# Performance work log

Hardware: AMD Instinct MI355X
Metric: run time of the kernel (lower is better)

## Reference

```python
import jax, jax.numpy as jnp
import numpy as np

D = 1024
H = 16
HD = D // H
S = 2048
B = 4
EPS = 1e-5


def gelu_tanh(x):
    c = jnp.sqrt(2.0 / jnp.pi).astype(x.dtype)
    return 0.5 * x * (1.0 + jnp.tanh(c * (x + 0.044715 * x ** 3)))


def layernorm(x, gamma, beta):
    mu = jnp.mean(x, axis=-1, keepdims=True)
    var = jnp.var(x, axis=-1, keepdims=True)
    return (x - mu) * jax.lax.rsqrt(var + EPS) * gamma + beta


def setup_inputs() -> dict:
    key = jax.random.key(0)
    ks = jax.random.split(key, 12)
    s = 0.02
    return {
        "x": jax.random.normal(ks[0], (B, S, D), jnp.float32),
        "Wq": jax.random.normal(ks[1], (D, D), jnp.float32) * s,
        "Wk": jax.random.normal(ks[2], (D, D), jnp.float32) * s,
        "Wv": jax.random.normal(ks[3], (D, D), jnp.float32) * s,
        "Wo": jax.random.normal(ks[4], (D, D), jnp.float32) * s,
        "bo": jnp.zeros((D,), jnp.float32),
        "W1": jax.random.normal(ks[5], (D, 4 * D), jnp.float32) * s,
        "b1": jnp.zeros((4 * D,), jnp.float32),
        "W2": jax.random.normal(ks[6], (4 * D, D), jnp.float32) * s,
        "b2": jnp.zeros((D,), jnp.float32),
        "g1": jnp.ones((D,), jnp.float32),
        "be1": jnp.zeros((D,), jnp.float32),
        "g2": jnp.ones((D,), jnp.float32),
        "be2": jnp.zeros((D,), jnp.float32),
    }


def reference(x, Wq, Wk, Wv, Wo, bo, W1, b1, W2, b2, g1, be1, g2, be2):
    b, n, d = x.shape
    # --- attention sub-block (pre-LN) ---
    h = layernorm(x, g1, be1)
    q = (h @ Wq).reshape(b, n, H, HD).transpose(0, 2, 1, 3)  # [b,H,n,hd]
    k = (h @ Wk).reshape(b, n, H, HD).transpose(0, 2, 1, 3)
    v = (h @ Wv).reshape(b, n, H, HD).transpose(0, 2, 1, 3)
    scores = jnp.einsum('bhqd,bhkd->bhqk', q, k) / jnp.sqrt(jnp.float32(HD))
    causal = jnp.tril(jnp.ones((n, n), dtype=bool))
    scores = jnp.where(causal, scores, -jnp.inf)
    w = jax.nn.softmax(scores, axis=-1)  # dropout rate 0 -> identity
    attn = jnp.einsum('bhqk,bhkd->bhqd', w, v)
    attn = attn.transpose(0, 2, 1, 3).reshape(b, n, d)
    x = x + (attn @ Wo + bo)
    # --- FFN sub-block (pre-LN) ---
    h = layernorm(x, g2, be2)
    h = gelu_tanh(h @ W1 + b1) @ W2 + b2
    return x + h
```

## Files before the change

### kernel.cpp

```cpp
#include <hip/hip_runtime.h>
#include <hip/hip_bf16.h>
#include <math.h>


typedef __attribute__((ext_vector_type(8))) short bf16x8;
typedef __attribute__((ext_vector_type(4))) float f32x4;

#define AS1 __attribute__((address_space(1)))
#define AS3 __attribute__((address_space(3)))

__device__ __forceinline__ void gl_lds16(const void* g, void* l) {
  __builtin_amdgcn_global_load_lds((const AS1 void*)g, (AS3 void*)l, 16, 0, 0);
}

__device__ __forceinline__ float gelu_f(float x) {
  const float c = 0.7978845608028654f;
  const float y = c * (x + 0.044715f * x * x * x);
  const float ay = fabsf(y);
  const float e = __expf(-2.0f * ay);
  float t = (1.0f - e) / (1.0f + e);
  t = copysignf(t, y);
  return 0.5f * x * (1.0f + t);
}

__device__ __forceinline__ float bf2f(short s) {
  unsigned u = ((unsigned)(unsigned short)s) << 16;
  return __builtin_bit_cast(float, u);
}
__device__ __forceinline__ short f2bf(float f) {
  __hip_bfloat16 h = __float2bfloat16(f);
  return __builtin_bit_cast(short, h);
}

__global__ void __launch_bounds__(256) tcvt_all(
    const float* __restrict__ Wq, const float* __restrict__ Wk,
    const float* __restrict__ Wv, const float* __restrict__ Wo,
    const float* __restrict__ W1, const float* __restrict__ W2,
    __hip_bfloat16* __restrict__ WqkvT, __hip_bfloat16* __restrict__ WoT,
    __hip_bfloat16* __restrict__ W1T, __hip_bfloat16* __restrict__ W2T) {
  __shared__ float t[32][33];
  const int bid = blockIdx.x;
  const float* W;
  __hip_bfloat16* WT;
  int K, N, n0, k0;
  if (bid < 4096) {
    const int which = bid >> 10, r = bid & 1023;
    K = 1024; N = 1024;
    n0 = (r & 31) * 32; k0 = (r >> 5) * 32;
    W = which == 0 ? Wq : which == 1 ? Wk : which == 2 ? Wv : Wo;
    WT = which < 3 ? WqkvT + which * 1024 * 1024 : WoT;
  } else if (bid < 8192) {
    const int r = bid - 4096;
    K = 1024; N = 4096;
    n0 = (r & 127) * 32; k0 = (r >> 7) * 32;
    W = W1; WT = W1T;
  } else {
    const int r = bid - 8192;
    K = 4096; N = 1024;
    n0 = (r & 31) * 32; k0 = (r >> 5) * 32;
    W = W2; WT = W2T;
  }
  const int tx = threadIdx.x, ty0 = threadIdx.y;
#pragma unroll
  for (int i = 0; i < 4; i++) {
    int ty = ty0 + i * 8;
    t[ty][tx] = W[(size_t)(k0 + ty) * N + n0 + tx];
  }
  __syncthreads();
#pragma unroll
  for (int i = 0; i < 4; i++) {
    int ty = ty0 + i * 8;
    WT[(size_t)(n0 + ty) * K + k0 + tx] = __float2bfloat16(t[tx][ty]);
  }
}

__global__ void __launch_bounds__(256) vtr_kernel(
    const __hip_bfloat16* __restrict__ qkv, __hip_bfloat16* __restrict__ vt) {
  __shared__ __hip_bfloat16 t[32][33];
  const int s0 = blockIdx.x * 32;
  const int hd0 = blockIdx.y * 32;
  const int bh = blockIdx.z;
  const int b = bh >> 4, h = bh & 15;
  const int tx = threadIdx.x, ty0 = threadIdx.y;
  const __hip_bfloat16* src =
      qkv + (size_t)(b * 2048 + s0) * 3072 + 2048 + h * 64 + hd0;
#pragma unroll
  for (int i = 0; i < 4; i++) {
    int ty = ty0 + i * 8;
    t[ty][tx] = src[(size_t)ty * 3072 + tx];
  }
  __syncthreads();
  __hip_bfloat16* dst = vt + ((size_t)bh * 64 + hd0) * 2048 + s0;
#pragma unroll
  for (int i = 0; i < 4; i++) {
    int ty = ty0 + i * 8;
    dst[(size_t)ty * 2048 + tx] = t[tx][ty];
  }
}

__global__ void __launch_bounds__(256) ln_kernel(
    const float* __restrict__ x, const float* __restrict__ gma,
    const float* __restrict__ bta, __hip_bfloat16* __restrict__ out) {
  const int row = blockIdx.x;
  const int tid = threadIdx.x;
  const float4 v = ((const float4*)(x + (size_t)row * 1024))[tid];
  float s = v.x + v.y + v.z + v.w;
  float s2 = v.x * v.x + v.y * v.y + v.z * v.z + v.w * v.w;
#pragma unroll
  for (int m = 32; m; m >>= 1) {
    s += __shfl_xor(s, m);
    s2 += __shfl_xor(s2, m);
  }
  __shared__ float red[8];
  const int w = tid >> 6, lane = tid & 63;
  if (lane == 0) { red[w] = s; red[4 + w] = s2; }
  __syncthreads();
  s = red[0] + red[1] + red[2] + red[3];
  s2 = red[4] + red[5] + red[6] + red[7];
  const float mu = s * (1.0f / 1024.0f);
  const float var = s2 * (1.0f / 1024.0f) - mu * mu;
  const float rs = rsqrtf(var + 1e-5f);
  const float4 gv = ((const float4*)gma)[tid];
  const float4 bv = ((const float4*)bta)[tid];
  __hip_bfloat16* orow = out + (size_t)row * 1024 + tid * 4;
  orow[0] = __float2bfloat16((v.x - mu) * rs * gv.x + bv.x);
  orow[1] = __float2bfloat16((v.y - mu) * rs * gv.y + bv.y);
  orow[2] = __float2bfloat16((v.z - mu) * rs * gv.z + bv.z);
  orow[3] = __float2bfloat16((v.w - mu) * rs * gv.w + bv.w);
}

__global__ void __launch_bounds__(256) ln_bf16_kernel(
    const __hip_bfloat16* __restrict__ x, const float* __restrict__ gma,
    const float* __restrict__ bta, __hip_bfloat16* __restrict__ out) {
  const int row = blockIdx.x;
  const int tid = threadIdx.x;
  const short4 raw = ((const short4*)(x + (size_t)row * 1024))[tid];
  const float v0 = bf2f(raw.x), v1 = bf2f(raw.y), v2 = bf2f(raw.z),
              v3 = bf2f(raw.w);
  float s = v0 + v1 + v2 + v3;
  float s2 = v0 * v0 + v1 * v1 + v2 * v2 + v3 * v3;
#pragma unroll
  for (int m = 32; m; m >>= 1) {
    s += __shfl_xor(s, m);
    s2 += __shfl_xor(s2, m);
  }
  __shared__ float red[8];
  const int w = tid >> 6, lane = tid & 63;
  if (lane == 0) { red[w] = s; red[4 + w] = s2; }
  __syncthreads();
  s = red[0] + red[1] + red[2] + red[3];
  s2 = red[4] + red[5] + red[6] + red[7];
  const float mu = s * (1.0f / 1024.0f);
  const float var = s2 * (1.0f / 1024.0f) - mu * mu;
  const float rs = rsqrtf(var + 1e-5f);
  const float4 gv = ((const float4*)gma)[tid];
  const float4 bv = ((const float4*)bta)[tid];
  __hip_bfloat16* orow = out + (size_t)row * 1024 + tid * 4;
  orow[0] = __float2bfloat16((v0 - mu) * rs * gv.x + bv.x);
  orow[1] = __float2bfloat16((v1 - mu) * rs * gv.y + bv.y);
  orow[2] = __float2bfloat16((v2 - mu) * rs * gv.z + bv.z);
  orow[3] = __float2bfloat16((v3 - mu) * rs * gv.w + bv.w);
}

template <int BM, int BN, int EPI>
__global__ void __launch_bounds__(512, 2) gemm8(
    const __hip_bfloat16* __restrict__ Ap, const __hip_bfloat16* __restrict__ Bp,
    void* __restrict__ outp, const float* __restrict__ bias,
    const float* __restrict__ resid, int N, int K) {
  constexpr int PM = BM / 2;
  constexpr int MR = PM / 16;
  constexpr int NPH = MR / 2;
  constexpr int HA = BM / 128;
  constexpr int ABYTES = BM * 128;
  constexpr int BUFB = ABYTES + BN * 128;
  __shared__ __attribute__((aligned(128))) char smem[2 * BUFB];

  const int tid = threadIdx.x;
  const int lane = tid & 63, w = tid >> 6;
  const int wr = w >> 2, wc = w & 3;
  const int cr = lane & 15, g = lane >> 4;

  const int gx = gridDim.x;
  const int nwg = gx * gridDim.y;
  const int orig = blockIdx.y * gx + blockIdx.x;
  const int f = (orig & 7) * (nwg >> 3) + (orig >> 3);
  const int sid = f >> 4, wit = f & 15;
  const int stm = gx >> 2;
  const int bm = (sid % stm) * 4 + (wit & 3);
  const int bn = (sid / stm) * 4 + (wit >> 2);
  const int bmr = bm * BM, bnr = bn * BN;
  const int nkt = K >> 6;

  const int srow8 = lane >> 3;
  const int ssl = ((lane & 7) ^ srow8) * 8;
  unsigned aofs[2][2], bofs[2][2];
#pragma unroll
  for (int h = 0; h < 2; h++)
#pragma unroll
    for (int c = 0; c < 2; c++) {
      const int ha = (h < HA) ? h : 0;
      aofs[h][c] =
          (unsigned)(((bmr + ha * 128 + (w + c * 8) * 8 + srow8) * K + ssl) * 2);
      bofs[h][c] =
          (unsigned)(((bnr + h * 128 + (w + c * 8) * 8 + srow8) * K + ssl) * 2);
    }

  const int rk = cr & 7;
  const char* aP[2][2];
  const char* bP[2][2];
#pragma unroll
  for (int bf = 0; bf < 2; bf++)
#pragma unroll
    for (int ks = 0; ks < 2; ks++) {
      aP[bf][ks] =
          smem + bf * BUFB + (wr * PM + cr) * 128 + ((ks * 4 + g) ^ rk) * 16;
      bP[bf][ks] = smem + bf * BUFB + ABYTES + (wc * 64 + cr) * 128 +
                   ((ks * 4 + g) ^ rk) * 16;
    }

#define STG_A(BUF, tt, h)                                                     \
  do {                                                                        \
    const unsigned col = (unsigned)(tt) * 128u;                               \
    gl_lds16((const char*)Ap + aofs[h][0] + col,                              \
             smem + (BUF) * BUFB + (h) * 16384 + w * 1024);                   \
    gl_lds16((const char*)Ap + aofs[h][1] + col,                              \
             smem + (BUF) * BUFB + (h) * 16384 + (w + 8) * 1024);             \
  } while (0)
#define STG_B(BUF, tt, h)                                                     \
  do {                                                                        \
    const unsigned col = (unsigned)(tt) * 128u;                               \
    gl_lds16((const char*)Bp + bofs[h][0] + col,                              \
             smem + (BUF) * BUFB + ABYTES + (h) * 16384 + w * 1024);          \
    gl_lds16((const char*)Bp + bofs[h][1] + col,                              \
             smem + (BUF) * BUFB + ABYTES + (h) * 16384 + (w + 8) * 1024);    \
  } while (0)

  f32x4 acc[MR][4];
#pragma unroll
  for (int i = 0; i < MR; i++)
#pragma unroll
    for (int j = 0; j < 4; j++) acc[i][j] = (f32x4){0.f, 0.f, 0.f, 0.f};
  bf16x8 bv[4][2];

#pragma unroll
  for (int h = 0; h < HA; h++) STG_A(0, 0, h);
  STG_B(0, 0, 0); STG_B(0, 0, 1);
  STG_B(1, 1, 0); STG_B(1, 1, 1);

#define TILE_BODY(BUF, t)                                                     \
  {                                                                           \
    asm volatile("s_waitcnt vmcnt(4)" ::: "memory");                          \
    __builtin_amdgcn_s_barrier();                                             \
    const int tA = ((t) + 1 < nkt) ? (t) + 1 : (t) - 1;                       \
    const int tB = ((t) + 2 < nkt) ? (t) + 2 : (t);                           \
    _Pragma("unroll") for (int q = 0; q < NPH; q++) {                         \
      bf16x8 av[2][2];                                                        \
      _Pragma("unroll") for (int mm = 0; mm < 2; mm++)                        \
          _Pragma("unroll") for (int ks = 0; ks < 2; ks++) av[mm][ks] =       \
          *(const bf16x8*)(aP[BUF][ks] + (q * 2 + mm) * 2048);                \
      if (q == 0) {                                                           \
        _Pragma("unroll") for (int n = 0; n < 4; n++)                         \
            _Pragma("unroll") for (int ks = 0; ks < 2; ks++) bv[n][ks] =      \
            *(const bf16x8*)(bP[BUF][ks] + n * 2048);                         \
      }                                                                       \
      if constexpr (NPH == 4) {                                               \
        if (q == 0) { STG_A((BUF) ^ 1, tA, 0); }                              \
        else if (q == 1) { STG_A((BUF) ^ 1, tA, 1); }                         \
        else if (q == 2) { STG_B(BUF, tB, 0); }                               \
        else { STG_B(BUF, tB, 1); }                                           \
      } else {                                                                \
        if (q == 0) { STG_A((BUF) ^ 1, tA, 0); }                              \
        else { STG_B(BUF, tB, 0); STG_B(BUF, tB, 1); }                        \
      }                                                                       \
      __builtin_amdgcn_s_barrier();                                           \
      asm volatile("s_waitcnt lgkmcnt(0)" ::: "memory");                      \
      __builtin_amdgcn_s_setprio(1);                                          \
      _Pragma("unroll") for (int mm = 0; mm < 2; mm++)                        \
          _Pragma("unroll") for (int n = 0; n < 4; n++)                       \
              _Pragma("unroll") for (int ks = 0; ks < 2; ks++)                \
                  acc[q * 2 + mm][n] =                                        \
          __builtin_amdgcn_mfma_f32_16x16x32_bf16(av[mm][ks], bv[n][ks],      \
                                                  acc[q * 2 + mm][n], 0, 0, 0); \
      __builtin_amdgcn_s_setprio(0);                                          \
    }                                                                         \
  }

  for (int t = 0; t < nkt; t += 2) {
    TILE_BODY(0, t)
    TILE_BODY(1, t + 1)
  }
  asm volatile("s_waitcnt vmcnt(0)" ::: "memory");

#pragma unroll
  for (int m = 0; m < MR; m++) {
#pragma unroll
    for (int rr = 0; rr < 4; rr++) {
      const int row = bmr + wr * PM + m * 16 + g * 4 + rr;
#pragma unroll
      for (int n = 0; n < 4; n++) {
        const int col = bnr + wc * 64 + n * 16 + cr;
        float v = acc[m][n][rr];
        if (EPI == 0) {
          ((__hip_bfloat16*)outp)[(size_t)row * N + col] = __float2bfloat16(v);
        } else if (EPI == 2) {
          v = gelu_f(v + bias[col]);
          ((__hip_bfloat16*)outp)[(size_t)row * N + col] = __float2bfloat16(v);
        } else {
          v += bias[col] + resid[(size_t)row * N + col];
          ((__hip_bfloat16*)outp)[(size_t)row * N + col] = __float2bfloat16(v);
        }
      }
    }
  }
#undef STG_A
#undef STG_B
#undef TILE_BODY
}

template <int EPI>
__global__ void __launch_bounds__(256) gemm97(
    const __hip_bfloat16* __restrict__ Ap, const __hip_bfloat16* __restrict__ Bp,
    void* __restrict__ outp, const float* __restrict__ bias,
    const void* __restrict__ resid, int N, int K) {
  __shared__ __hip_bfloat16 sA[128 * 64];
  __shared__ __hip_bfloat16 sB[128 * 64];
  const int tid = threadIdx.x;
  const int lane = tid & 63, w = tid >> 6;
  const int wr = w >> 1, wc = w & 1;
  const int cr = lane & 15, g = lane >> 4;

  const int gx = gridDim.x;
  const int nwg = gx * gridDim.y;
  const int orig = blockIdx.y * gx + blockIdx.x;
  const int f = (orig & 7) * (nwg >> 3) + (orig >> 3);
  const int sid = f >> 4, wit = f & 15;
  const int stm = gx >> 2;
  const int bm = (sid % stm) * 4 + (wit & 3);
  const int bn = (sid / stm) * 4 + (wit >> 2);
  const int bmr = bm * 128, bnr = bn * 128;

  const int l8 = lane >> 3;
  const int ssl = ((lane & 7) ^ l8) * 8;
  const int rk = cr & 7;

  f32x4 acc[4][4];
#pragma unroll
  for (int i = 0; i < 4; i++)
#pragma unroll
    for (int j = 0; j < 4; j++) acc[i][j] = (f32x4){0.f, 0.f, 0.f, 0.f};

  for (int k0 = 0; k0 < K; k0 += 64) {
#pragma unroll
    for (int i = 0; i < 4; i++) {
      const int chunk = w * 4 + i;
      const int row = chunk * 8 + l8;
      gl_lds16(Ap + (size_t)(bmr + row) * K + k0 + ssl, sA + chunk * 512);
      gl_lds16(Bp + (size_t)(bnr + row) * K + k0 + ssl, sB + chunk * 512);
    }
    __syncthreads();
#pragma unroll
    for (int ks = 0; ks < 2; ks++) {
      bf16x8 a[4], b[4];
#pragma unroll
      for (int m = 0; m < 4; m++)
        a[m] = *(const bf16x8*)(sA + (wr * 64 + m * 16 + cr) * 64 +
                                ((ks * 4 + g) ^ rk) * 8);
#pragma unroll
      for (int n = 0; n < 4; n++)
        b[n] = *(const bf16x8*)(sB + (wc * 64 + n * 16 + cr) * 64 +
                                ((ks * 4 + g) ^ rk) * 8);
#pragma unroll
      for (int m = 0; m < 4; m++)
#pragma unroll
        for (int n = 0; n < 4; n++)
          acc[m][n] =
              __builtin_amdgcn_mfma_f32_16x16x32_bf16(a[m], b[n], acc[m][n], 0, 0, 0);
    }
    __syncthreads();
  }

#pragma unroll
  for (int m = 0; m < 4; m++) {
#pragma unroll
    for (int rr = 0; rr < 4; rr++) {
      const int row = bmr + wr * 64 + m * 16 + g * 4 + rr;
#pragma unroll
      for (int n = 0; n < 4; n++) {
        const int col = bnr + wc * 64 + n * 16 + cr;
        float v = acc[m][n][rr];
        if (EPI == 0) {
          ((__hip_bfloat16*)outp)[(size_t)row * N + col] = __float2bfloat16(v);
        } else if (EPI == 1) {
          v += bias[col] + ((const float*)resid)[(size_t)row * N + col];
          ((float*)outp)[(size_t)row * N + col] = v;
        } else {
          v += bias[col] +
               bf2f(((const short*)resid)[(size_t)row * N + col]);
          ((float*)outp)[(size_t)row * N + col] = v;
        }
      }
    }
  }
}

__global__ void __launch_bounds__(256) attn_kernel(
    const __hip_bfloat16* __restrict__ qkv, const __hip_bfloat16* __restrict__ vt,
    __hip_bfloat16* __restrict__ o) {
  __shared__ __hip_bfloat16 sK[2][64 * 64];
  __shared__ __hip_bfloat16 sV[2][64 * 64];
  __shared__ __hip_bfloat16 pl[4][16][64];
  const int tid = threadIdx.x, lane = tid & 63, w = tid >> 6;
  const int orig = blockIdx.x;
  const int f = (orig & 7) * 64 + (orig >> 3);
  const int bh = f >> 3;
  const int p = f & 7;
  const int b = bh >> 4, h = bh & 15;
  const int cr = lane & 15, g = lane >> 4;
  const float NEG = -1e30f;
  const float SC2 = 0.18033688011112042f;
  const int sw = cr & 7;
  const int sg0 = (g ^ sw) * 8;
  const int sg1 = ((g ^ sw) ^ 4) * 8;
  const int pkey = (cr & 7) << 1;

  bf16x8 vones;
#pragma unroll
  for (int j = 0; j < 8; j++) vones[j] = (short)0x3F80;

  const __hip_bfloat16* kbase = qkv + (size_t)(b * 2048) * 3072 + 1024 + h * 64;
  const __hip_bfloat16* vbase = vt + (size_t)bh * 64 * 2048;
  const int l8 = lane >> 3, c8 = lane & 7;
  const int c8s = (c8 ^ l8) * 8;
#define STAGE_TILE(bi, ktile)                                                   \
  {                                                                             \
    _Pragma("unroll") for (int i = 0; i < 2; i++) {                             \
      const int rb = (i * 4 + w) * 8 + l8;                                      \
      gl_lds16(kbase + (size_t)((ktile) * 64 + rb) * 3072 + c8s,                \
               &sK[bi][(i * 4 + w) * 512]);                                     \
      gl_lds16(vbase + (size_t)rb * 2048 + (ktile) * 64 + c8s,                  \
               &sV[bi][(i * 4 + w) * 512]);                                     \
    }                                                                           \
  }

  for (int seg = 0; seg < 2; ++seg) {
    const int qt = seg == 0 ? (15 - p) : p;
    const int qr0 = qt * 128 + w * 32;

    bf16x8 aq[2][2];
#pragma unroll
    for (int m = 0; m < 2; m++) {
      const __hip_bfloat16* qp =
          qkv + (size_t)(b * 2048 + qr0 + m * 16 + cr) * 3072 + h * 64 + g * 8;
      bf16x8 q0 = *(const bf16x8*)qp;
      bf16x8 q1 = *(const bf16x8*)(qp + 32);
#pragma unroll
      for (int j = 0; j < 8; j++) {
        aq[m][0][j] = f2bf(bf2f(q0[j]) * SC2);
        aq[m][1][j] = f2bf(bf2f(q1[j]) * SC2);
      }
    }

    f32x4 oacc[2][4];
    f32x4 lacc[2];
#pragma unroll
    for (int m = 0; m < 2; m++) {
#pragma unroll
      for (int i = 0; i < 4; i++) oacc[m][i] = (f32x4){0.f, 0.f, 0.f, 0.f};
      lacc[m] = (f32x4){0.f, 0.f, 0.f, 0.f};
    }

    const int nkt = (qt + 1) * 2;
    __syncthreads();
    STAGE_TILE(0, 0);
    asm volatile("s_waitcnt vmcnt(0)" ::: "memory");
    __syncthreads();
    int cur = 0;

    for (int kt = 0; kt < nkt; ++kt) {
      if (kt + 1 < nkt) STAGE_TILE(cur ^ 1, kt + 1);

      if (kt * 64 <= qr0 + 31) {
        f32x4 st[4][2];
        __builtin_amdgcn_s_setprio(1);
#pragma unroll
        for (int kf = 0; kf < 4; kf++) {
          const bf16x8 bk0 = *(const bf16x8*)&sK[cur][(kf * 16 + cr) * 64 + sg0];
          const bf16x8 bk1 = *(const bf16x8*)&sK[cur][(kf * 16 + cr) * 64 + sg1];
#pragma unroll
          for (int mq = 0; mq < 2; mq++) {
            f32x4 z = (f32x4){0.f, 0.f, 0.f, 0.f};
            z = __builtin_amdgcn_mfma_f32_16x16x32_bf16(bk0, aq[mq][0], z, 0, 0, 0);
            z = __builtin_amdgcn_mfma_f32_16x16x32_bf16(bk1, aq[mq][1], z, 0, 0, 0);
            st[kf][mq] = z;
          }
        }
        __builtin_amdgcn_s_setprio(0);
        if (kt * 64 + 63 > qr0) {
#pragma unroll
          for (int kf = 0; kf < 4; kf++)
#pragma unroll
            for (int mq = 0; mq < 2; mq++)
#pragma unroll
              for (int rr = 0; rr < 4; rr++) {
                const int kvcol = kt * 64 + kf * 16 + g * 4 + rr;
                const int qrow = qr0 + mq * 16 + cr;
                if (kvcol > qrow) st[kf][mq][rr] = NEG;
              }
        }
        bf16x8 bvv0[4], bvv1[4];
#pragma unroll
        for (int nf = 0; nf < 4; nf++) {
          bvv0[nf] = *(const bf16x8*)&sV[cur][(nf * 16 + cr) * 64 + sg0];
          bvv1[nf] = *(const bf16x8*)&sV[cur][(nf * 16 + cr) * 64 + sg1];
        }
#pragma unroll
        for (int mq = 0; mq < 2; mq++) {
#pragma unroll
          for (int kf = 0; kf < 4; kf++) {
            unsigned pb[4];
#pragma unroll
            for (int rr = 0; rr < 4; rr++) {
              const float pv = exp2f(st[kf][mq][rr]);
              pb[rr] = __builtin_bit_cast(unsigned, pv) & 0xFFFF0000u;
            }
            uint2 pk;
            pk.x = pb[1] | (pb[0] >> 16);
            pk.y = pb[3] | (pb[2] >> 16);
            const int slot4 = (kf * 4 + g) ^ pkey;
            *(uint2*)&pl[w][cr][slot4 * 4] = pk;
          }
          const bf16x8 pa0 = *(const bf16x8*)&pl[w][cr][((2 * g) ^ pkey) * 4];
          const bf16x8 pa1 = *(const bf16x8*)&pl[w][cr][((2 * g + 8) ^ pkey) * 4];
          __builtin_amdgcn_s_setprio(1);
#pragma unroll
          for (int nf = 0; nf < 4; nf++) {
            oacc[mq][nf] = __builtin_amdgcn_mfma_f32_16x16x32_bf16(pa0, bvv0[nf], oacc[mq][nf], 0, 0, 0);
            oacc[mq][nf] = __builtin_amdgcn_mfma_f32_16x16x32_bf16(pa1, bvv1[nf], oacc[mq][nf], 0, 0, 0);
          }
          lacc[mq] = __builtin_amdgcn_mfma_f32_16x16x32_bf16(pa0, vones, lacc[mq], 0, 0, 0);
          lacc[mq] = __builtin_amdgcn_mfma_f32_16x16x32_bf16(pa1, vones, lacc[mq], 0, 0, 0);
          __builtin_amdgcn_s_setprio(0);
        }
      }

      if (kt + 1 < nkt) {
        asm volatile("s_waitcnt vmcnt(0)" ::: "memory");
        __syncthreads();
        cur ^= 1;
      }
    }

#pragma unroll
    for (int m = 0; m < 2; m++) {
      float il[4];
#pragma unroll
      for (int rr = 0; rr < 4; rr++)
        il[rr] = 1.0f / lacc[m][rr];
#pragma unroll
      for (int nf = 0; nf < 4; nf++)
#pragma unroll
        for (int rr = 0; rr < 4; rr++) {
          const int row = qr0 + m * 16 + g * 4 + rr;
          o[(size_t)(b * 2048 + row) * 1024 + h * 64 + nf * 16 + cr] =
              __float2bfloat16(oacc[m][nf][rr] * il[rr]);
        }
    }
  }
#undef STAGE_TILE
}

extern "C" void kernel_launch(void* const* d_in, const int* in_sizes, int n_in,
                              void* d_out, int out_size, void* d_ws, size_t ws_size,
                              hipStream_t stream) {
  const float* x   = (const float*)d_in[0];
  const float* Wq  = (const float*)d_in[1];
  const float* Wk  = (const float*)d_in[2];
  const float* Wv  = (const float*)d_in[3];
  const float* Wo  = (const float*)d_in[4];
  const float* bo  = (const float*)d_in[5];
  const float* W1  = (const float*)d_in[6];
  const float* b1  = (const float*)d_in[7];
  const float* W2  = (const float*)d_in[8];
  const float* b2  = (const float*)d_in[9];
  const float* g1  = (const float*)d_in[10];
  const float* be1 = (const float*)d_in[11];
  const float* g2  = (const float*)d_in[12];
  const float* be2 = (const float*)d_in[13];

  char* ws = (char*)d_ws;
  const size_t MB = 1024 * 1024;
  __hip_bfloat16* hA    = (__hip_bfloat16*)(ws + 0);
  __hip_bfloat16* attnO = (__hip_bfloat16*)(ws + 0);
  __hip_bfloat16* qkv   = (__hip_bfloat16*)(ws + 16 * MB);
  __hip_bfloat16* x2b   = (__hip_bfloat16*)(ws + 16 * MB);
  __hip_bfloat16* h2    = (__hip_bfloat16*)(ws + 48 * MB);
  __hip_bfloat16* vtg   = (__hip_bfloat16*)(ws + 64 * MB);
  __hip_bfloat16* act   = (__hip_bfloat16*)(ws + 64 * MB);
  __hip_bfloat16* WqkvT = (__hip_bfloat16*)(ws + 128 * MB);
  __hip_bfloat16* WoT   = (__hip_bfloat16*)(ws + 134 * MB);
  __hip_bfloat16* W1T   = (__hip_bfloat16*)(ws + 136 * MB);
  __hip_bfloat16* W2T   = (__hip_bfloat16*)(ws + 144 * MB);

  const dim3 tb(32, 8);
  tcvt_all<<<12288, tb, 0, stream>>>(Wq, Wk, Wv, Wo, W1, W2,
                                     WqkvT, WoT, W1T, W2T);

  ln_kernel<<<8192, 256, 0, stream>>>(x, g1, be1, hA);
  gemm8<128, 256, 0><<<dim3(64, 12), 512, 0, stream>>>(
      hA, WqkvT, qkv, nullptr, nullptr, 3072, 1024);
  vtr_kernel<<<dim3(64, 2, 64), tb, 0, stream>>>(qkv, vtg);
  attn_kernel<<<512, 256, 0, stream>>>(qkv, vtg, attnO);
  gemm8<128, 256, 3><<<dim3(64, 4), 512, 0, stream>>>(
      attnO, WoT, x2b, bo, x, 1024, 1024);
  ln_bf16_kernel<<<8192, 256, 0, stream>>>(x2b, g2, be2, h2);
  gemm8<256, 256, 2><<<dim3(32, 16), 512, 0, stream>>>(
      h2, W1T, act, b1, nullptr, 4096, 1024);
  gemm97<4><<<dim3(64, 8), 256, 0, stream>>>(
      act, W2T, (float*)d_out, b2, x2b, 1024, 4096);
  (void)in_sizes; (void)n_in; (void)out_size; (void)ws_size;
}
```

Baseline: 364.1 us.

## Fuse V transpose into QKV GEMM epilogue and move W1 GEMM to gemm97

The QKV projection GEMM now writes the V part directly in transposed [b, hd, s] layout from its accumulators, using packed 4-element stores, so the separate vtr_kernel launch and its extra read/write of V go away. The FFN up-projection with GELU is also switched from the 512-thread gemm8<256,256> kernel to the 256-thread gemm97 kernel with a GELU epilogue. That swap changes the tile shape and grid for the largest GEMM and could help or hurt its throughput. The transposed stores are strided across rows of the output, so they may coalesce poorly.

```diff
diff --git a/kernel.cpp b/kernel.cpp
--- a/kernel.cpp
+++ b/kernel.cpp
@@ -74,30 +74,6 @@
   }
 }
 
-__global__ void __launch_bounds__(256) vtr_kernel(
-    const __hip_bfloat16* __restrict__ qkv, __hip_bfloat16* __restrict__ vt) {
-  __shared__ __hip_bfloat16 t[32][33];
-  const int s0 = blockIdx.x * 32;
-  const int hd0 = blockIdx.y * 32;
-  const int bh = blockIdx.z;
-  const int b = bh >> 4, h = bh & 15;
-  const int tx = threadIdx.x, ty0 = threadIdx.y;
-  const __hip_bfloat16* src =
-      qkv + (size_t)(b * 2048 + s0) * 3072 + 2048 + h * 64 + hd0;
-#pragma unroll
-  for (int i = 0; i < 4; i++) {
-    int ty = ty0 + i * 8;
-    t[ty][tx] = src[(size_t)ty * 3072 + tx];
-  }
-  __syncthreads();
-  __hip_bfloat16* dst = vt + ((size_t)bh * 64 + hd0) * 2048 + s0;
-#pragma unroll
-  for (int i = 0; i < 4; i++) {
-    int ty = ty0 + i * 8;
-    dst[(size_t)ty * 2048 + tx] = t[tx][ty];
-  }
-}
-
 __global__ void __launch_bounds__(256) ln_kernel(
     const float* __restrict__ x, const float* __restrict__ gma,
     const float* __restrict__ bta, __hip_bfloat16* __restrict__ out) {
@@ -166,7 +142,8 @@
 __global__ void __launch_bounds__(512, 2) gemm8(
     const __hip_bfloat16* __restrict__ Ap, const __hip_bfloat16* __restrict__ Bp,
     void* __restrict__ outp, const float* __restrict__ bias,
-    const float* __restrict__ resid, int N, int K) {
+    const float* __restrict__ resid, int N, int K,
+    __hip_bfloat16* __restrict__ vtp) {
   constexpr int PM = BM / 2;
   constexpr int MR = PM / 16;
   constexpr int NPH = MR / 2;
@@ -291,6 +268,26 @@
   }
   asm volatile("s_waitcnt vmcnt(0)" ::: "memory");
 
+  if (EPI == 5 && bnr >= 2048) {
+    const int bq = bmr >> 11;
+    const int sbase = (bmr & 2047) + wr * PM + g * 4;
+#pragma unroll
+    for (int m = 0; m < MR; m++) {
+      const int s0 = sbase + m * 16;
+#pragma unroll
+      for (int n = 0; n < 4; n++) {
+        const int hdg = bnr - 2048 + wc * 64 + n * 16 + cr;
+        short4 pk;
+        pk.x = f2bf(acc[m][n][0]);
+        pk.y = f2bf(acc[m][n][1]);
+        pk.z = f2bf(acc[m][n][2]);
+        pk.w = f2bf(acc[m][n][3]);
+        *(short4*)&vtp[((size_t)bq * 1024 + hdg) * 2048 + s0] = pk;
+      }
+    }
+    return;
+  }
+
 #pragma unroll
   for (int m = 0; m < MR; m++) {
 #pragma unroll
@@ -300,10 +297,7 @@
       for (int n = 0; n < 4; n++) {
         const int col = bnr + wc * 64 + n * 16 + cr;
         float v = acc[m][n][rr];
-        if (EPI == 0) {
-          ((__hip_bfloat16*)outp)[(size_t)row * N + col] = __float2bfloat16(v);
-        } else if (EPI == 2) {
-          v = gelu_f(v + bias[col]);
+        if (EPI == 0 || EPI == 5) {
           ((__hip_bfloat16*)outp)[(size_t)row * N + col] = __float2bfloat16(v);
         } else {
           v += bias[col] + resid[(size_t)row * N + col];
@@ -390,9 +384,9 @@
         float v = acc[m][n][rr];
         if (EPI == 0) {
           ((__hip_bfloat16*)outp)[(size_t)row * N + col] = __float2bfloat16(v);
-        } else if (EPI == 1) {
-          v += bias[col] + ((const float*)resid)[(size_t)row * N + col];
-          ((float*)outp)[(size_t)row * N + col] = v;
+        } else if (EPI == 2) {
+          v = gelu_f(v + bias[col]);
+          ((__hip_bfloat16*)outp)[(size_t)row * N + col] = __float2bfloat16(v);
         } else {
           v += bias[col] +
                bf2f(((const short*)resid)[(size_t)row * N + col]);
@@ -606,14 +600,13 @@
                                      WqkvT, WoT, W1T, W2T);
 
   ln_kernel<<<8192, 256, 0, stream>>>(x, g1, be1, hA);
-  gemm8<128, 256, 0><<<dim3(64, 12), 512, 0, stream>>>(
-      hA, WqkvT, qkv, nullptr, nullptr, 3072, 1024);
-  vtr_kernel<<<dim3(64, 2, 64), tb, 0, stream>>>(qkv, vtg);
+  gemm8<128, 256, 5><<<dim3(64, 12), 512, 0, stream>>>(
+      hA, WqkvT, qkv, nullptr, nullptr, 3072, 1024, vtg);
   attn_kernel<<<512, 256, 0, stream>>>(qkv, vtg, attnO);
   gemm8<128, 256, 3><<<dim3(64, 4), 512, 0, stream>>>(
-      attnO, WoT, x2b, bo, x, 1024, 1024);
+      attnO, WoT, x2b, bo, x, 1024, 1024, nullptr);
   ln_bf16_kernel<<<8192, 256, 0, stream>>>(x2b, g2, be2, h2);
-  gemm8<256, 256, 2><<<dim3(32, 16), 512, 0, stream>>>(
+  gemm97<2><<<dim3(64, 32), 256, 0, stream>>>(
       h2, W1T, act, b1, nullptr, 4096, 1024);
   gemm97<4><<<dim3(64, 8), 256, 0, stream>>>(
       act, W2T, (float*)d_out, b2, x2b, 1024, 4096);
```

Result: slower. 378.0 us (+3.8%).
